# Optimization experiments

Measured on AMD Instinct MI355X. Metric: run time of the kernel, lower is better.

## Reference

```python
import jax, jax.numpy as jnp
import numpy as np

N = 50000
E = 500000
D = 128      # input_nf = output_nf = hidden_nf
EPS = 1e-8
MAX_TRANS = 10.0


def setup_inputs() -> dict:
    key = jax.random.key(0)
    ks = jax.random.split(key, 16)
    s = lambda k, shp: jax.random.normal(k, shp, dtype=jnp.float32) * 0.05
    inp = {
        "h": jax.random.normal(ks[0], (N, D), dtype=jnp.float32),
        "edge_index": jax.random.randint(ks[1], (2, E), 0, N, dtype=jnp.int64),
        "coord": jax.random.normal(ks[2], (N, 3), dtype=jnp.float32),
        # edge_mlp: Linear(2D+1 -> D), SiLU, Linear(D -> D), SiLU
        "We1": s(ks[3], (2 * D + 1, D)), "be1": jnp.zeros((D,), jnp.float32),
        "We2": s(ks[4], (D, D)),         "be2": jnp.zeros((D,), jnp.float32),
        # att_mlp: Linear(D -> 1), Sigmoid
        "Watt": s(ks[5], (D, 1)), "batt": jnp.zeros((1,), jnp.float32),
        # coord_mlp: Linear(D -> D), SiLU, Linear(D -> 1, bias=False, xavier gain=0.001)
        "Wc1": s(ks[6], (D, D)), "bc1": jnp.zeros((D,), jnp.float32),
        "Wc2": s(ks[7], (D, 1)) * 0.001,
        # node_mlp: Linear(2D -> D), SiLU, Linear(D -> D)
        "Wn1": s(ks[8], (2 * D, D)), "bn1": jnp.zeros((D,), jnp.float32),
        "Wn2": s(ks[9], (D, D)),     "bn2": jnp.zeros((D,), jnp.float32),
    }
    return inp


def _segment_mean(data, seg_ids, num_segments):
    tot = jax.ops.segment_sum(data, seg_ids, num_segments=num_segments)
    cnt = jax.ops.segment_sum(jnp.ones_like(data), seg_ids, num_segments=num_segments)
    return tot / jnp.clip(cnt, 1.0, None)


def reference(h, edge_index, coord, We1, be1, We2, be2, Watt, batt,
              Wc1, bc1, Wc2, Wn1, bn1, Wn2, bn2):
    row, col = edge_index[0], edge_index[1]

    # coord2radial (normalize=False)
    coord_diff = coord[row] - coord[col]                      # [E, 3]
    radial = jnp.sum(coord_diff ** 2, axis=1, keepdims=True)  # [E, 1]

    # edge_model with attention
    e_in = jnp.concatenate([h[row], h[col], radial], axis=1)  # [E, 2D+1]
    e = jax.nn.silu(e_in @ We1 + be1)
    edge_feat = jax.nn.silu(e @ We2 + be2)                    # [E, D]
    att = jax.nn.sigmoid(edge_feat @ Watt + batt)             # [E, 1]
    edge_feat = edge_feat * att

    # coord_model (update_coords=True, coords_agg='mean', tanh=False)
    cw = jax.nn.silu(edge_feat @ Wc1 + bc1) @ Wc2             # [E, 1]
    trans = jnp.clip(coord_diff * cw, -MAX_TRANS, MAX_TRANS)  # [E, 3]
    agg_c = jnp.clip(_segment_mean(trans, row, N), -MAX_TRANS, MAX_TRANS)
    coord_out = coord + agg_c

    # node_model (residual=True)
    agg = jax.ops.segment_sum(edge_feat, row, num_segments=N)  # [N, D]
    n_in = jnp.concatenate([h, agg], axis=1)                   # [N, 2D]
    h_out = h + (jax.nn.silu(n_in @ Wn1 + bn1) @ Wn2 + bn2)

    return h_out, coord_out, edge_feat
```

## Files before the change

kernel.cpp:

```cpp
#include <hip/hip_runtime.h>

typedef unsigned short ushort_t;
typedef __attribute__((ext_vector_type(8))) short short8;
typedef __attribute__((ext_vector_type(4))) short short4v;
typedef __attribute__((ext_vector_type(4))) float f32x4;

#define NN 50000
#define EE 500000
#define DD 128
#define MAXT 10.0f

#define MFMA(a,b,c) __builtin_amdgcn_mfma_f32_16x16x32_bf16((a),(b),(c),0,0,0)

__device__ __forceinline__ ushort_t f2bf(float x){
  unsigned u = __float_as_uint(x);
  u += 0x7FFFu + ((u>>16)&1u);
  return (ushort_t)(u>>16);
}
__device__ __forceinline__ float bf2f(ushort_t u){
  return __uint_as_float(((unsigned)u)<<16);
}
__device__ __forceinline__ float sigm(float x){ return 1.0f/(1.0f+__expf(-x)); }
__device__ __forceinline__ float siluf(float x){ return x*sigm(x); }
__device__ __forceinline__ float clamp10(float x){ return fminf(fmaxf(x,-MAXT),MAXT); }

__device__ __forceinline__ short8 ldcvt(const float* p){
  f32x4 x = *(const f32x4*)p;
  f32x4 y = *(const f32x4*)(p+4);
  short8 t;
  #pragma unroll
  for (int j=0;j<4;++j){ t[j]=(short)f2bf(x[j]); t[j+4]=(short)f2bf(y[j]); }
  return t;
}

__global__ void k_prep(const float* __restrict__ We1, const float* __restrict__ We2,
                       const float* __restrict__ Wc1, const float* __restrict__ Wn1,
                       const float* __restrict__ Wn2, ushort_t* __restrict__ wpre)
{
  int idx = blockIdx.x*256 + threadIdx.x;
  if (idx >= 7*16384) return;
  int mat = idx >> 14;
  int loc = idx & 16383;
  int n = loc >> 7;
  int kidx = loc & 127;
  int ko = 16*(kidx&7) + (kidx>>3);
  float v;
  switch(mat){
    case 0: v = We1[kidx*DD + n]; break;
    case 1: v = We1[(128+kidx)*DD + n]; break;
    case 2: v = We2[kidx*DD + n]; break;
    case 3: v = Wc1[ko*DD + n]; break;
    case 4: v = Wn1[kidx*DD + n]; break;
    case 5: v = Wn1[(128+kidx)*DD + n]; break;
    default: v = Wn2[ko*DD + n]; break;
  }
  int byteoff = n*256 + ((kidx*2) ^ ((n&7)<<4));
  *(ushort_t*)((char*)wpre + (size_t)mat*32768 + byteoff) = f2bf(v);
}

__global__ void k_count(const int* __restrict__ eidx, int* __restrict__ cnt){
  int e = blockIdx.x*256 + threadIdx.x;
  if (e < EE) atomicAdd(&cnt[eidx[e]], 1);
}
#define SCAN_B 196
__global__ void k_bsum(const int* __restrict__ cnt, int* __restrict__ bsum){
  __shared__ int sh[256];
  int t = threadIdx.x;
  int i = blockIdx.x*256 + t;
  sh[t] = (i < NN) ? cnt[i] : 0;
  __syncthreads();
  for (int off=128; off>0; off>>=1){
    if (t < off) sh[t] += sh[t+off];
    __syncthreads();
  }
  if (t==0) bsum[blockIdx.x] = sh[0];
}
__global__ void k_bscan(const int* __restrict__ bsum, int* __restrict__ boff){
  __shared__ int sh[256];
  int t = threadIdx.x;
  sh[t] = (t < SCAN_B) ? bsum[t] : 0;
  __syncthreads();
  for (int off=1; off<256; off<<=1){
    int x = (t>=off) ? sh[t-off] : 0;
    __syncthreads();
    sh[t] += x;
    __syncthreads();
  }
  if (t < SCAN_B) boff[t] = (t>0) ? sh[t-1] : 0;
}
__global__ void k_rscan(const int* __restrict__ cnt, const int* __restrict__ boff,
                        int* __restrict__ rowstart, int* __restrict__ cursor){
  __shared__ int sh[256];
  int t = threadIdx.x;
  int i = blockIdx.x*256 + t;
  int v = (i < NN) ? cnt[i] : 0;
  sh[t] = v;
  __syncthreads();
  for (int off=1; off<256; off<<=1){
    int x = (t>=off) ? sh[t-off] : 0;
    __syncthreads();
    sh[t] += x;
    __syncthreads();
  }
  int excl = sh[t] - v + boff[blockIdx.x];
  if (i < NN){ rowstart[i] = excl; cursor[i] = excl; }
  if (i == 0) rowstart[NN] = EE;
}
__global__ void k_scatter(const int* __restrict__ eidx, int* __restrict__ cursor,
                          int* __restrict__ csr){
  int e = blockIdx.x*256 + threadIdx.x;
  if (e < EE){
    int p = atomicAdd(&cursor[eidx[e]], 1);
    csr[p] = e;
  }
}

__device__ __forceinline__ void stage(const ushort_t* __restrict__ wpre, int mat,
                                      ushort_t* Wbuf, int tid)
{
  const f32x4* src = (const f32x4*)(wpre + (size_t)mat*16384);
  f32x4* dst = (f32x4*)Wbuf;
  #pragma unroll
  for (int i=0;i<4;++i) dst[tid + 512*i] = src[tid + 512*i];
}
__device__ __forceinline__ void zacc(f32x4 acc[2][4]){
  #pragma unroll
  for (int i=0;i<2;++i)
    #pragma unroll
    for (int j=0;j<4;++j) acc[i][j] = (f32x4){0.f,0.f,0.f,0.f};
}
__device__ __forceinline__ void gemm_b16(const short8 af[2][4], const ushort_t* Wbuf,
                                         int cbase, int q, int s, f32x4 acc[2][4])
{
  #pragma unroll
  for (int kc=0;kc<4;++kc){
    const int koff = ((kc*64+q*16) ^ ((s&7)<<4));
    #pragma unroll
    for (int ct=0;ct<4;++ct){
      short8 bf = *(const short8*)((const char*)Wbuf + (cbase+ct*16+s)*256 + koff);
      acc[0][ct] = MFMA(af[0][kc],bf,acc[0][ct]);
      acc[1][ct] = MFMA(af[1][kc],bf,acc[1][ct]);
    }
  }
}
__device__ __forceinline__ void gemm_lds16(const ushort_t* ebuf, const ushort_t* Wbuf,
                                           int mbase, int cbase, int q, int s,
                                           f32x4 acc[2][4])
{
  #pragma unroll
  for (int kc=0;kc<4;++kc){
    const int koff = ((kc*64+q*16) ^ ((s&7)<<4));
    short8 a0 = *(const short8*)((const char*)ebuf + (mbase+s)*256 + koff);
    short8 a1 = *(const short8*)((const char*)ebuf + (mbase+16+s)*256 + koff);
    #pragma unroll
    for (int ct=0;ct<4;++ct){
      short8 bf = *(const short8*)((const char*)Wbuf + (cbase+ct*16+s)*256 + koff);
      acc[0][ct] = MFMA(a0,bf,acc[0][ct]);
      acc[1][ct] = MFMA(a1,bf,acc[1][ct]);
    }
  }
}

__launch_bounds__(512,4)
__global__ void k_pre1(const float* __restrict__ h,
                       const ushort_t* __restrict__ wpre,
                       const float* __restrict__ be1,
                       ushort_t* __restrict__ H1a, ushort_t* __restrict__ H1b)
{
  __shared__ ushort_t Wbuf[16384];
  const int tid = threadIdx.x;
  const int wv = tid>>6, ln = tid&63;
  const int wm = wv&3, wn = wv>>2;
  const int q = ln>>4, s = ln&15;
  const int cbase = wn*64;
  const int n0 = blockIdx.x*128;
  const int mb = wm*32;
  const int nd0 = min(n0 + mb + s,      NN-1);
  const int nd1 = min(n0 + mb + 16 + s, NN-1);

  f32x4 acc[2][4];
  short8 af[2][4];
  zacc(acc);
  #pragma unroll
  for (int kc=0;kc<4;++kc){
    af[0][kc] = ldcvt(h + (size_t)nd0*DD + kc*32 + q*8);
    af[1][kc] = ldcvt(h + (size_t)nd1*DD + kc*32 + q*8);
  }
  stage(wpre, 0, Wbuf, tid);
  __syncthreads();
  gemm_b16(af, Wbuf, cbase, q, s, acc);
  {
    float bb[4];
    #pragma unroll
    for (int ct=0;ct<4;++ct) bb[ct]=be1[cbase+16*ct+s];
    #pragma unroll
    for (int mt=0;mt<2;++mt)
      #pragma unroll
      for (int r=0;r<4;++r){
        int n = n0 + mb + mt*16 + q*4 + r;
        if (n < NN){
          ushort_t* op = H1a + (size_t)n*DD + cbase + s;
          #pragma unroll
          for (int ct=0;ct<4;++ct) op[16*ct] = f2bf(acc[mt][ct][r] + bb[ct]);
        }
      }
  }
  zacc(acc);
  __syncthreads();
  stage(wpre, 1, Wbuf, tid);
  __syncthreads();
  gemm_b16(af, Wbuf, cbase, q, s, acc);
  {
    #pragma unroll
    for (int mt=0;mt<2;++mt)
      #pragma unroll
      for (int r=0;r<4;++r){
        int n = n0 + mb + mt*16 + q*4 + r;
        if (n < NN){
          ushort_t* op = H1b + (size_t)n*DD + cbase + s;
          #pragma unroll
          for (int ct=0;ct<4;++ct) op[16*ct] = f2bf(acc[mt][ct][r]);
        }
      }
  }
}

__launch_bounds__(512,4)
__global__ void k_edge(const ushort_t* __restrict__ H1a,
                       const ushort_t* __restrict__ H1b,
                       const int* __restrict__ eidx,
                       const float* __restrict__ coord,
                       const float* __restrict__ We1,
                       const float* __restrict__ be2,
                       const float* __restrict__ Watt,
                       const float* __restrict__ batt,
                       const float* __restrict__ bc1,
                       const float* __restrict__ Wc2,
                       const ushort_t* __restrict__ wpre,
                       float* __restrict__ ef_out,
                       float* __restrict__ trans)
{
  __shared__ ushort_t Wbuf[16384];
  __shared__ ushort_t ebuf[16384];
  __shared__ float dscr[128][2];
  const int tid = threadIdx.x;
  const int wv = tid>>6, ln = tid&63;
  const int wm = wv&3, wn = wv>>2;
  const int q = ln>>4, s = ln&15;
  const int cbase = wn*64;
  const int we0 = blockIdx.x*128;
  const int mb = wm*32;
  const int* rowI = eidx;
  const int* colI = eidx + EE;

  const int jg = we0 + mb + (ln&31);
  const int jgc = min(jg, EE-1);
  const int rg = rowI[jgc], cg = colI[jgc];
  const float cdx = coord[rg*3+0]-coord[cg*3+0];
  const float cdy = coord[rg*3+1]-coord[cg*3+1];
  const float cdz = coord[rg*3+2]-coord[cg*3+2];

  const int e0 = min(we0+mb+s,    EE-1);
  const int e1 = min(we0+mb+16+s, EE-1);
  const int r0 = rowI[e0], c0 = colI[e0];
  const int r1 = rowI[e1], c1 = colI[e1];
  float rad[2];
  { float dx=coord[r0*3+0]-coord[c0*3+0], dy=coord[r0*3+1]-coord[c0*3+1],
          dz=coord[r0*3+2]-coord[c0*3+2];
    rad[0]=dx*dx+dy*dy+dz*dz; }
  { float dx=coord[r1*3+0]-coord[c1*3+0], dy=coord[r1*3+1]-coord[c1*3+1],
          dz=coord[r1*3+2]-coord[c1*3+2];
    rad[1]=dx*dx+dy*dy+dz*dz; }

  stage(wpre, 2, Wbuf, tid);

  {
    float w[2][8];
    #pragma unroll
    for (int gi=0; gi<2; ++gi){
      const int g = wn*8 + q*2 + gi;
      const f32x4* pw = (const f32x4*)(We1 + 256*DD + g*8);
      f32x4 w0=pw[0], w1=pw[1];
      #pragma unroll
      for (int t=0;t<4;++t){ w[gi][t]=w0[t]; w[gi][t+4]=w1[t]; }
    }
    #pragma unroll
    for (int mt=0; mt<2; ++mt){
      const int nR = mt ? r1 : r0, nC = mt ? c1 : c0;
      const float rd = rad[mt];
      const int m = mb + mt*16 + s;
      #pragma unroll
      for (int gi=0; gi<2; ++gi){
        const int g = wn*8 + q*2 + gi;
        short8 sa = *(const short8*)(H1a + (size_t)nR*DD + g*8);
        short8 sb = *(const short8*)(H1b + (size_t)nC*DD + g*8);
        short8 pk;
        #pragma unroll
        for (int t=0;t<8;++t){
          float e = bf2f((ushort_t)sa[t]) + bf2f((ushort_t)sb[t]) + rd*w[gi][t];
          pk[t] = (short)f2bf(siluf(e));
        }
        *(short8*)((char*)ebuf + m*256 + ((g*16) ^ ((m&7)<<4))) = pk;
      }
    }
  }

  f32x4 acc[2][4];
  zacc(acc);
  __syncthreads();

  gemm_lds16(ebuf, Wbuf, mb, cbase, q, s, acc);
  {
    float wa[4], bb[4];
    #pragma unroll
    for (int ct=0;ct<4;++ct){ wa[ct]=Watt[cbase+16*ct+s]; bb[ct]=be2[cbase+16*ct+s]; }
    #pragma unroll
    for (int mt=0;mt<2;++mt){
      #pragma unroll
      for (int r=0;r<4;++r){
        float p = 0.f;
        #pragma unroll
        for (int ct=0;ct<4;++ct){
          float v = siluf(acc[mt][ct][r] + bb[ct]);
          acc[mt][ct][r] = v;
          p += v*wa[ct];
        }
        p += __shfl_xor(p,1); p += __shfl_xor(p,2);
        p += __shfl_xor(p,4); p += __shfl_xor(p,8);
        if (s==0) dscr[mb + mt*16 + q*4 + r][wn] = p;
      }
    }
  }
  __syncthreads();
  stage(wpre, 3, Wbuf, tid);
  {
    const float bat = batt[0];
    #pragma unroll
    for (int mt=0;mt<2;++mt){
      #pragma unroll
      for (int r=0;r<4;++r){
        int m = mb + mt*16 + q*4 + r;
        float att = sigm(dscr[m][0] + dscr[m][1] + bat);
        short4v pk;
        #pragma unroll
        for (int ct=0;ct<4;++ct){
          acc[mt][ct][r] *= att;
          pk[ct]=(short)f2bf(acc[mt][ct][r]);
        }
        *(short4v*)((char*)ebuf + m*256 + ((16*s+8*wn) ^ ((m&7)<<4))) = pk;
        int e = we0 + m;
        if (e < EE){
          float* rp = ef_out + (size_t)e*DD + cbase + s;
          #pragma unroll
          for (int ct=0;ct<4;++ct) rp[16*ct] = acc[mt][ct][r];
        }
      }
    }
  }
  zacc(acc);
  __syncthreads();

  gemm_lds16(ebuf, Wbuf, mb, cbase, q, s, acc);
  {
    float wc[4], bb[4];
    #pragma unroll
    for (int ct=0;ct<4;++ct){ wc[ct]=Wc2[cbase+16*ct+s]; bb[ct]=bc1[cbase+16*ct+s]; }
    #pragma unroll
    for (int mt=0;mt<2;++mt){
      #pragma unroll
      for (int r=0;r<4;++r){
        float p = 0.f;
        #pragma unroll
        for (int ct=0;ct<4;++ct) p += siluf(acc[mt][ct][r]+bb[ct])*wc[ct];
        p += __shfl_xor(p,1); p += __shfl_xor(p,2);
        p += __shfl_xor(p,4); p += __shfl_xor(p,8);
        if (s==0) dscr[mb + mt*16 + q*4 + r][wn] = p;
      }
    }
  }
  __syncthreads();
  if (wn==0 && ln<32 && jg < EE){
    float p = dscr[mb+ln][0] + dscr[mb+ln][1];
    trans[(size_t)jg*3+0] = clamp10(cdx*p);
    trans[(size_t)jg*3+1] = clamp10(cdy*p);
    trans[(size_t)jg*3+2] = clamp10(cdz*p);
  }
}

__launch_bounds__(256)
__global__ void k_agg(const float* __restrict__ ef,
                      const float* __restrict__ trans,
                      const int* __restrict__ rowstart,
                      const int* __restrict__ csr,
                      const float* __restrict__ coord,
                      ushort_t* __restrict__ aggb,
                      float* __restrict__ coord_out)
{
  const int wv = threadIdx.x>>6, ln = threadIdx.x&63;
  const int n = blockIdx.x*4 + wv;
  if (n >= NN) return;
  const int rs = rowstart[n], re = rowstart[n+1];
  const int deg = re - rs;
  const int half = ln>>5, l4 = (ln&31)*4;
  float a0=0,a1=0,a2=0,a3=0;
  for (int j=half; j<deg; j+=2){
    const float* p = ef + (size_t)csr[rs+j]*DD + l4;
    f32x4 v = *(const f32x4*)p;
    a0+=v[0]; a1+=v[1]; a2+=v[2]; a3+=v[3];
  }
  a0 += __shfl_xor(a0,32); a1 += __shfl_xor(a1,32);
  a2 += __shfl_xor(a2,32); a3 += __shfl_xor(a3,32);
  if (half==0){
    short4v o = { (short)f2bf(a0),(short)f2bf(a1),(short)f2bf(a2),(short)f2bf(a3) };
    *(short4v*)(aggb + (size_t)n*DD + l4) = o;
  }
  float tx=0,ty=0,tz=0;
  for (int j=ln;j<deg;j+=64){
    const float* t = trans + (size_t)csr[rs+j]*3;
    tx+=t[0]; ty+=t[1]; tz+=t[2];
  }
  #pragma unroll
  for (int m=1;m<64;m<<=1){
    tx+=__shfl_xor(tx,m); ty+=__shfl_xor(ty,m); tz+=__shfl_xor(tz,m);
  }
  if (ln==0){
    const float inv = 1.0f/(float)max(deg,1);
    coord_out[(size_t)n*3+0] = coord[(size_t)n*3+0] + clamp10(tx*inv);
    coord_out[(size_t)n*3+1] = coord[(size_t)n*3+1] + clamp10(ty*inv);
    coord_out[(size_t)n*3+2] = coord[(size_t)n*3+2] + clamp10(tz*inv);
  }
}

__launch_bounds__(512,4)
__global__ void k_node(const float* __restrict__ h,
                       const ushort_t* __restrict__ aggb,
                       const ushort_t* __restrict__ wpre,
                       const float* __restrict__ bn1,
                       const float* __restrict__ bn2,
                       float* __restrict__ hout)
{
  __shared__ ushort_t Wbuf[16384];
  __shared__ ushort_t ubuf[16384];
  const int tid = threadIdx.x;
  const int wv = tid>>6, ln = tid&63;
  const int wm = wv&3, wn = wv>>2;
  const int q = ln>>4, s = ln&15;
  const int cbase = wn*64;
  const int n0 = blockIdx.x*128;
  const int mb = wm*32;
  const int nd0 = min(n0 + mb + s,      NN-1);
  const int nd1 = min(n0 + mb + 16 + s, NN-1);

  f32x4 acc[2][4];
  short8 af[2][4];
  zacc(acc);

  #pragma unroll
  for (int kc=0;kc<4;++kc){
    af[0][kc] = ldcvt(h + (size_t)nd0*DD + kc*32 + q*8);
    af[1][kc] = ldcvt(h + (size_t)nd1*DD + kc*32 + q*8);
  }
  stage(wpre, 4, Wbuf, tid);
  __syncthreads();
  gemm_b16(af, Wbuf, cbase, q, s, acc);

  #pragma unroll
  for (int kc=0;kc<4;++kc){
    af[0][kc] = *(const short8*)(aggb + (size_t)nd0*DD + kc*32 + q*8);
    af[1][kc] = *(const short8*)(aggb + (size_t)nd1*DD + kc*32 + q*8);
  }
  __syncthreads();
  stage(wpre, 5, Wbuf, tid);
  __syncthreads();
  gemm_b16(af, Wbuf, cbase, q, s, acc);

  {
    float bb[4];
    #pragma unroll
    for (int ct=0;ct<4;++ct) bb[ct]=bn1[cbase+16*ct+s];
    #pragma unroll
    for (int mt=0;mt<2;++mt){
      #pragma unroll
      for (int r=0;r<4;++r){
        int m = mb + mt*16 + q*4 + r;
        short4v pk;
        #pragma unroll
        for (int ct=0;ct<4;++ct) pk[ct]=(short)f2bf(siluf(acc[mt][ct][r]+bb[ct]));
        *(short4v*)((char*)ubuf + m*256 + ((16*s+8*wn) ^ ((m&7)<<4))) = pk;
      }
    }
  }
  zacc(acc);
  __syncthreads();
  stage(wpre, 6, Wbuf, tid);
  __syncthreads();

  gemm_lds16(ubuf, Wbuf, mb, cbase, q, s, acc);

  {
    float bb[4];
    #pragma unroll
    for (int ct=0;ct<4;++ct) bb[ct]=bn2[cbase+16*ct+s];
    #pragma unroll
    for (int mt=0;mt<2;++mt){
      #pragma unroll
      for (int r=0;r<4;++r){
        int n = n0 + mb + mt*16 + q*4 + r;
        if (n < NN){
          const float* hp = h + (size_t)n*DD + cbase + s;
          float* op = hout + (size_t)n*DD + cbase + s;
          #pragma unroll
          for (int ct=0;ct<4;++ct) op[16*ct] = hp[16*ct] + acc[mt][ct][r] + bb[ct];
        }
      }
    }
  }
}

extern "C" void kernel_launch(void* const* d_in, const int* in_sizes, int n_in,
                              void* d_out, int out_size, void* d_ws, size_t ws_size,
                              hipStream_t stream)
{
  const float* h    = (const float*)d_in[0];
  const int*   eidx = (const int*)  d_in[1];
  const float* coord= (const float*)d_in[2];
  const float* We1  = (const float*)d_in[3];
  const float* be1  = (const float*)d_in[4];
  const float* We2  = (const float*)d_in[5];
  const float* be2  = (const float*)d_in[6];
  const float* Watt = (const float*)d_in[7];
  const float* batt = (const float*)d_in[8];
  const float* Wc1  = (const float*)d_in[9];
  const float* bc1  = (const float*)d_in[10];
  const float* Wc2  = (const float*)d_in[11];
  const float* Wn1  = (const float*)d_in[12];
  const float* bn1  = (const float*)d_in[13];
  const float* Wn2  = (const float*)d_in[14];
  const float* bn2  = (const float*)d_in[15];

  float* hout     = (float*)d_out;
  float* coordout = hout + (size_t)NN*DD;
  float* efout    = coordout + (size_t)NN*3;

  char* ws = (char*)d_ws;
  float*    trans = (float*)(ws);
  ushort_t* aggb  = (ushort_t*)(ws + 6000000);
  int*   cnt      = (int*)  (ws + 18800000);
  int*   cursor   = (int*)  (ws + 19000000);
  int*   rowstart = (int*)  (ws + 19200000);
  int*   csr      = (int*)  (ws + 19400064);
  ushort_t* wpre  = (ushort_t*)(ws + 21400064);
  ushort_t* H1a   = (ushort_t*)(ws + 21629440);
  ushort_t* H1b   = (ushort_t*)(ws + 34429440);
  int*   bsum     = csr;
  int*   boff     = csr + 256;

  hipMemsetAsync(cnt, 0, 200000, stream);
  k_prep   <<<448, 256, 0, stream>>>(We1, We2, Wc1, Wn1, Wn2, wpre);
  k_count  <<<1954,256, 0, stream>>>(eidx, cnt);
  k_bsum   <<<196, 256, 0, stream>>>(cnt, bsum);
  k_bscan  <<<1,   256, 0, stream>>>(bsum, boff);
  k_rscan  <<<196, 256, 0, stream>>>(cnt, boff, rowstart, cursor);
  k_scatter<<<1954,256, 0, stream>>>(eidx, cursor, csr);
  k_pre1   <<<391, 512, 0, stream>>>(h, wpre, be1, H1a, H1b);
  k_edge   <<<3907,512, 0, stream>>>(H1a, H1b, eidx, coord, We1, be2, Watt,
                                     batt, bc1, Wc2, wpre, efout, trans);
  k_agg    <<<12500,256,0, stream>>>(efout, trans, rowstart, csr, coord, aggb, coordout);
  k_node   <<<391, 512, 0, stream>>>(h, aggb, wpre, bn1, bn2, hout);
}
```

Baseline: 627.2 us.

## Fuse CSR build, pre-GEMM and aggregation+node kernels to cut launches

Several kernels are merged to cut launch count and intermediate traffic. Weight prep and degree counting run as one launch. The three-kernel scan becomes a single pass that claims per-block bases with a global atomic. The CSR scatter shares a launch with the first node GEMM. Edge-feature aggregation now runs inside the node-MLP kernel and writes straight to LDS instead of a bf16 global buffer. The trade-off is that the gather now has far fewer blocks, each walking several nodes in a serial loop, which may expose memory latency. The atomic-based scan also makes row offsets depend on block order.

New measurement: 662.1 us. +5.6%, slower.

```diff
diff --git a/kernel.cpp b/kernel.cpp
--- a/kernel.cpp
+++ b/kernel.cpp
@@ -33,52 +33,46 @@
   return t;
 }
 
-__global__ void k_prep(const float* __restrict__ We1, const float* __restrict__ We2,
-                       const float* __restrict__ Wc1, const float* __restrict__ Wn1,
-                       const float* __restrict__ Wn2, ushort_t* __restrict__ wpre)
-{
-  int idx = blockIdx.x*256 + threadIdx.x;
-  if (idx >= 7*16384) return;
-  int mat = idx >> 14;
-  int loc = idx & 16383;
-  int n = loc >> 7;
-  int kidx = loc & 127;
-  int ko = 16*(kidx&7) + (kidx>>3);
-  float v;
-  switch(mat){
-    case 0: v = We1[kidx*DD + n]; break;
-    case 1: v = We1[(128+kidx)*DD + n]; break;
-    case 2: v = We2[kidx*DD + n]; break;
-    case 3: v = Wc1[ko*DD + n]; break;
-    case 4: v = Wn1[kidx*DD + n]; break;
-    case 5: v = Wn1[(128+kidx)*DD + n]; break;
-    default: v = Wn2[ko*DD + n]; break;
-  }
-  int byteoff = n*256 + ((kidx*2) ^ ((n&7)<<4));
-  *(ushort_t*)((char*)wpre + (size_t)mat*32768 + byteoff) = f2bf(v);
-}
-
-__global__ void k_count(const int* __restrict__ eidx, int* __restrict__ cnt){
-  int e = blockIdx.x*256 + threadIdx.x;
-  if (e < EE) atomicAdd(&cnt[eidx[e]], 1);
-}
-#define SCAN_B 196
-__global__ void k_bsum(const int* __restrict__ cnt, int* __restrict__ bsum){
+__global__ void k_prep_count(const float* __restrict__ We1, const float* __restrict__ We2,
+                             const float* __restrict__ Wc1, const float* __restrict__ Wn1,
+                             const float* __restrict__ Wn2, ushort_t* __restrict__ wpre,
+                             const int* __restrict__ eidx, int* __restrict__ cnt)
+{
+  if (blockIdx.x < 448){
+    int idx = blockIdx.x*256 + threadIdx.x;
+    if (idx >= 7*16384) return;
+    int mat = idx >> 14;
+    int loc = idx & 16383;
+    int n = loc >> 7;
+    int kidx = loc & 127;
+    int ko = 16*(kidx&7) + (kidx>>3);
+    float v;
+    switch(mat){
+      case 0: v = We1[kidx*DD + n]; break;
+      case 1: v = We1[(128+kidx)*DD + n]; break;
+      case 2: v = We2[kidx*DD + n]; break;
+      case 3: v = Wc1[ko*DD + n]; break;
+      case 4: v = Wn1[kidx*DD + n]; break;
+      case 5: v = Wn1[(128+kidx)*DD + n]; break;
+      default: v = Wn2[ko*DD + n]; break;
+    }
+    int byteoff = n*256 + ((kidx*2) ^ ((n&7)<<4));
+    *(ushort_t*)((char*)wpre + (size_t)mat*32768 + byteoff) = f2bf(v);
+  } else {
+    int e = (blockIdx.x-448)*256 + threadIdx.x;
+    if (e < EE) atomicAdd(&cnt[eidx[e]], 1);
+  }
+}
+
+__global__ void k_offsets(const int* __restrict__ cnt, int* __restrict__ gbase,
+                          int* __restrict__ rowstart, int* __restrict__ cursor)
+{
   __shared__ int sh[256];
+  __shared__ int base;
   int t = threadIdx.x;
   int i = blockIdx.x*256 + t;
-  sh[t] = (i < NN) ? cnt[i] : 0;
-  __syncthreads();
-  for (int off=128; off>0; off>>=1){
-    if (t < off) sh[t] += sh[t+off];
-    __syncthreads();
-  }
-  if (t==0) bsum[blockIdx.x] = sh[0];
-}
-__global__ void k_bscan(const int* __restrict__ bsum, int* __restrict__ boff){
-  __shared__ int sh[256];
-  int t = threadIdx.x;
-  sh[t] = (t < SCAN_B) ? bsum[t] : 0;
+  int v = (i < NN) ? cnt[i] : 0;
+  sh[t] = v;
   __syncthreads();
   for (int off=1; off<256; off<<=1){
     int x = (t>=off) ? sh[t-off] : 0;
@@ -86,33 +80,10 @@
     sh[t] += x;
     __syncthreads();
   }
-  if (t < SCAN_B) boff[t] = (t>0) ? sh[t-1] : 0;
-}
-__global__ void k_rscan(const int* __restrict__ cnt, const int* __restrict__ boff,
-                        int* __restrict__ rowstart, int* __restrict__ cursor){
-  __shared__ int sh[256];
-  int t = threadIdx.x;
-  int i = blockIdx.x*256 + t;
-  int v = (i < NN) ? cnt[i] : 0;
-  sh[t] = v;
-  __syncthreads();
-  for (int off=1; off<256; off<<=1){
-    int x = (t>=off) ? sh[t-off] : 0;
-    __syncthreads();
-    sh[t] += x;
-    __syncthreads();
-  }
-  int excl = sh[t] - v + boff[blockIdx.x];
+  if (t == 255) base = atomicAdd(gbase, sh[255]);
+  __syncthreads();
+  int excl = sh[t] - v + base;
   if (i < NN){ rowstart[i] = excl; cursor[i] = excl; }
-  if (i == 0) rowstart[NN] = EE;
-}
-__global__ void k_scatter(const int* __restrict__ eidx, int* __restrict__ cursor,
-                          int* __restrict__ csr){
-  int e = blockIdx.x*256 + threadIdx.x;
-  if (e < EE){
-    int p = atomicAdd(&cursor[eidx[e]], 1);
-    csr[p] = e;
-  }
 }
 
 __device__ __forceinline__ void stage(const ushort_t* __restrict__ wpre, int mat,
@@ -162,12 +133,22 @@
 }
 
 __launch_bounds__(512,4)
-__global__ void k_pre1(const float* __restrict__ h,
-                       const ushort_t* __restrict__ wpre,
-                       const float* __restrict__ be1,
-                       ushort_t* __restrict__ H1a, ushort_t* __restrict__ H1b)
+__global__ void k_scatter_pre1(const int* __restrict__ eidx, int* __restrict__ cursor,
+                               int* __restrict__ csr,
+                               const float* __restrict__ h,
+                               const ushort_t* __restrict__ wpre,
+                               const float* __restrict__ be1,
+                               ushort_t* __restrict__ H1a, ushort_t* __restrict__ H1b)
 {
   __shared__ ushort_t Wbuf[16384];
+  if (blockIdx.x >= 391){
+    int e = (blockIdx.x-391)*512 + threadIdx.x;
+    if (e < EE){
+      int p = atomicAdd(&cursor[eidx[e]], 1);
+      csr[p] = e;
+    }
+    return;
+  }
   const int tid = threadIdx.x;
   const int wv = tid>>6, ln = tid&63;
   const int wm = wv&3, wn = wv>>2;
@@ -387,60 +368,22 @@
   }
 }
 
-__launch_bounds__(256)
-__global__ void k_agg(const float* __restrict__ ef,
-                      const float* __restrict__ trans,
-                      const int* __restrict__ rowstart,
-                      const int* __restrict__ csr,
-                      const float* __restrict__ coord,
-                      ushort_t* __restrict__ aggb,
-                      float* __restrict__ coord_out)
-{
-  const int wv = threadIdx.x>>6, ln = threadIdx.x&63;
-  const int n = blockIdx.x*4 + wv;
-  if (n >= NN) return;
-  const int rs = rowstart[n], re = rowstart[n+1];
-  const int deg = re - rs;
-  const int half = ln>>5, l4 = (ln&31)*4;
-  float a0=0,a1=0,a2=0,a3=0;
-  for (int j=half; j<deg; j+=2){
-    const float* p = ef + (size_t)csr[rs+j]*DD + l4;
-    f32x4 v = *(const f32x4*)p;
-    a0+=v[0]; a1+=v[1]; a2+=v[2]; a3+=v[3];
-  }
-  a0 += __shfl_xor(a0,32); a1 += __shfl_xor(a1,32);
-  a2 += __shfl_xor(a2,32); a3 += __shfl_xor(a3,32);
-  if (half==0){
-    short4v o = { (short)f2bf(a0),(short)f2bf(a1),(short)f2bf(a2),(short)f2bf(a3) };
-    *(short4v*)(aggb + (size_t)n*DD + l4) = o;
-  }
-  float tx=0,ty=0,tz=0;
-  for (int j=ln;j<deg;j+=64){
-    const float* t = trans + (size_t)csr[rs+j]*3;
-    tx+=t[0]; ty+=t[1]; tz+=t[2];
-  }
-  #pragma unroll
-  for (int m=1;m<64;m<<=1){
-    tx+=__shfl_xor(tx,m); ty+=__shfl_xor(ty,m); tz+=__shfl_xor(tz,m);
-  }
-  if (ln==0){
-    const float inv = 1.0f/(float)max(deg,1);
-    coord_out[(size_t)n*3+0] = coord[(size_t)n*3+0] + clamp10(tx*inv);
-    coord_out[(size_t)n*3+1] = coord[(size_t)n*3+1] + clamp10(ty*inv);
-    coord_out[(size_t)n*3+2] = coord[(size_t)n*3+2] + clamp10(tz*inv);
-  }
-}
-
 __launch_bounds__(512,4)
-__global__ void k_node(const float* __restrict__ h,
-                       const ushort_t* __restrict__ aggb,
-                       const ushort_t* __restrict__ wpre,
-                       const float* __restrict__ bn1,
-                       const float* __restrict__ bn2,
-                       float* __restrict__ hout)
+__global__ void k_aggnode(const float* __restrict__ h,
+                          const float* __restrict__ ef,
+                          const float* __restrict__ trans,
+                          const int* __restrict__ cnt,
+                          const int* __restrict__ rowstart,
+                          const int* __restrict__ csr,
+                          const float* __restrict__ coord,
+                          const ushort_t* __restrict__ wpre,
+                          const float* __restrict__ bn1,
+                          const float* __restrict__ bn2,
+                          float* __restrict__ hout,
+                          float* __restrict__ coord_out)
 {
   __shared__ ushort_t Wbuf[16384];
-  __shared__ ushort_t ubuf[16384];
+  __shared__ ushort_t abuf[16384];
   const int tid = threadIdx.x;
   const int wv = tid>>6, ln = tid&63;
   const int wm = wv&3, wn = wv>>2;
@@ -451,6 +394,35 @@
   const int nd0 = min(n0 + mb + s,      NN-1);
   const int nd1 = min(n0 + mb + 16 + s, NN-1);
 
+  {
+    const int hw = tid>>5;
+    const int l  = tid&31;
+    #pragma unroll 1
+    for (int c=0; c<8; ++c){
+      const int m = hw*8 + c;
+      const int n = n0 + m;
+      float a0=0.f,a1=0.f,a2=0.f,a3=0.f,ts=0.f;
+      if (n < NN){
+        const int rs = rowstart[n];
+        const int deg = cnt[n];
+        for (int j=0;j<deg;++j){
+          const int e = csr[rs+j];
+          f32x4 v = *(const f32x4*)(ef + (size_t)e*DD + l*4);
+          a0+=v[0]; a1+=v[1]; a2+=v[2]; a3+=v[3];
+          if (l<3) ts += trans[(size_t)e*3 + l];
+        }
+        if (l<3){
+          float inv = 1.0f/(float)max(deg,1);
+          coord_out[(size_t)n*3+l] = coord[(size_t)n*3+l] + clamp10(ts*inv);
+        }
+      }
+      short4v pk = {(short)f2bf(a0),(short)f2bf(a1),(short)f2bf(a2),(short)f2bf(a3)};
+      *(short4v*)((char*)abuf + m*256 + (((l>>1)*16) ^ ((m&7)<<4)) + (l&1)*8) = pk;
+    }
+  }
+  stage(wpre, 4, Wbuf, tid);
+  __syncthreads();
+
   f32x4 acc[2][4];
   short8 af[2][4];
   zacc(acc);
@@ -460,20 +432,21 @@
     af[0][kc] = ldcvt(h + (size_t)nd0*DD + kc*32 + q*8);
     af[1][kc] = ldcvt(h + (size_t)nd1*DD + kc*32 + q*8);
   }
-  stage(wpre, 4, Wbuf, tid);
-  __syncthreads();
   gemm_b16(af, Wbuf, cbase, q, s, acc);
 
   #pragma unroll
   for (int kc=0;kc<4;++kc){
-    af[0][kc] = *(const short8*)(aggb + (size_t)nd0*DD + kc*32 + q*8);
-    af[1][kc] = *(const short8*)(aggb + (size_t)nd1*DD + kc*32 + q*8);
+    const int koff = (kc*64+q*16) ^ ((s&7)<<4);
+    af[0][kc] = *(const short8*)((const char*)abuf + (mb+s)*256 + koff);
+    af[1][kc] = *(const short8*)((const char*)abuf + (mb+16+s)*256 + koff);
   }
   __syncthreads();
   stage(wpre, 5, Wbuf, tid);
   __syncthreads();
   gemm_b16(af, Wbuf, cbase, q, s, acc);
-
+  __syncthreads();
+
+  stage(wpre, 6, Wbuf, tid);
   {
     float bb[4];
     #pragma unroll
@@ -486,16 +459,14 @@
         short4v pk;
         #pragma unroll
         for (int ct=0;ct<4;++ct) pk[ct]=(short)f2bf(siluf(acc[mt][ct][r]+bb[ct]));
-        *(short4v*)((char*)ubuf + m*256 + ((16*s+8*wn) ^ ((m&7)<<4))) = pk;
+        *(short4v*)((char*)abuf + m*256 + ((16*s+8*wn) ^ ((m&7)<<4))) = pk;
       }
     }
   }
   zacc(acc);
   __syncthreads();
-  stage(wpre, 6, Wbuf, tid);
-  __syncthreads();
-
-  gemm_lds16(ubuf, Wbuf, mb, cbase, q, s, acc);
+
+  gemm_lds16(abuf, Wbuf, mb, cbase, q, s, acc);
 
   {
     float bb[4];
@@ -544,27 +515,21 @@
 
   char* ws = (char*)d_ws;
   float*    trans = (float*)(ws);
-  ushort_t* aggb  = (ushort_t*)(ws + 6000000);
-  int*   cnt      = (int*)  (ws + 18800000);
-  int*   cursor   = (int*)  (ws + 19000000);
-  int*   rowstart = (int*)  (ws + 19200000);
-  int*   csr      = (int*)  (ws + 19400064);
-  ushort_t* wpre  = (ushort_t*)(ws + 21400064);
-  ushort_t* H1a   = (ushort_t*)(ws + 21629440);
-  ushort_t* H1b   = (ushort_t*)(ws + 34429440);
-  int*   bsum     = csr;
-  int*   boff     = csr + 256;
-
-  hipMemsetAsync(cnt, 0, 200000, stream);
-  k_prep   <<<448, 256, 0, stream>>>(We1, We2, Wc1, Wn1, Wn2, wpre);
-  k_count  <<<1954,256, 0, stream>>>(eidx, cnt);
-  k_bsum   <<<196, 256, 0, stream>>>(cnt, bsum);
-  k_bscan  <<<1,   256, 0, stream>>>(bsum, boff);
-  k_rscan  <<<196, 256, 0, stream>>>(cnt, boff, rowstart, cursor);
-  k_scatter<<<1954,256, 0, stream>>>(eidx, cursor, csr);
-  k_pre1   <<<391, 512, 0, stream>>>(h, wpre, be1, H1a, H1b);
-  k_edge   <<<3907,512, 0, stream>>>(H1a, H1b, eidx, coord, We1, be2, Watt,
-                                     batt, bc1, Wc2, wpre, efout, trans);
-  k_agg    <<<12500,256,0, stream>>>(efout, trans, rowstart, csr, coord, aggb, coordout);
-  k_node   <<<391, 512, 0, stream>>>(h, aggb, wpre, bn1, bn2, hout);
-}
+  int*   cnt      = (int*)  (ws + 6000000);
+  int*   gbase    = (int*)  (ws + 6200000);
+  int*   cursor   = (int*)  (ws + 6200064);
+  int*   rowstart = (int*)  (ws + 6400064);
+  int*   csr      = (int*)  (ws + 6600064);
+  ushort_t* wpre  = (ushort_t*)(ws + 8600064);
+  ushort_t* H1a   = (ushort_t*)(ws + 8829440);
+  ushort_t* H1b   = (ushort_t*)(ws + 21629440);
+
+  hipMemsetAsync(cnt, 0, 200064, stream);
+  k_prep_count  <<<2402,256, 0, stream>>>(We1, We2, Wc1, Wn1, Wn2, wpre, eidx, cnt);
+  k_offsets     <<<196, 256, 0, stream>>>(cnt, gbase, rowstart, cursor);
+  k_scatter_pre1<<<1368,512, 0, stream>>>(eidx, cursor, csr, h, wpre, be1, H1a, H1b);
+  k_edge        <<<3907,512, 0, stream>>>(H1a, H1b, eidx, coord, We1, be2, Watt,
+                                          batt, bc1, Wc2, wpre, efout, trans);
+  k_aggnode     <<<391, 512, 0, stream>>>(h, efout, trans, cnt, rowstart, csr,
+                                          coord, wpre, bn1, bn2, hout, coordout);
+}
```
